# Kernel tuning notes

Measured on AMD Instinct MI355X. Metric: run time of the kernel, lower is better.

The kernel has to match this reference:

```python
import jax, jax.numpy as jnp
import numpy as np

S = 32   # parent grid side
G = 64   # child grid side (2*S)
C = 16   # channels
DN = ('NDHWC', 'DHWIO', 'NDHWC')


def conv3(t, w, b):
    # t: [D,H,W,Cin] dense grid; zero padding == nonexistent coords contribute 0 (ME semantics)
    return jax.lax.conv_general_dilated(t[None], w, (1, 1, 1), 'SAME', dimension_numbers=DN)[0] + b


def _grids():
    ix = jnp.arange(G)
    px = (ix % 2)[:, None, None]
    py = (ix % 2)[None, :, None]
    pz = (ix % 2)[None, None, :]
    oct_m = {(a, b, c): (px == a) & (py == b) & (pz == c)
             for a in (0, 1) for b in (0, 1) for c in (0, 1)}
    groups6 = [[(0, 0, 0)], [(1, 1, 0)], [(1, 0, 1)], [(0, 1, 1)],
               [(1, 0, 0), (0, 1, 0)], [(0, 0, 1), (1, 1, 1)]]
    g6 = [jnp.any(jnp.stack([oct_m[o] for o in g]), 0) for g in groups6]
    s3 = (ix // 2)[:, None, None] + (ix // 2)[None, :, None] + (ix // 2)[None, None, :]
    m3 = [(s3 % 3) == j for j in range(3)]  # 3-way repartition (group_mask_gen_par)
    return g6, m3


def coder(feat, occ, w1, b1, w2, b2):
    # ProbCoder: conv -> ReLU -> conv -> sigmoid; outputs exist only at input coords
    of = occ[..., None].astype(feat.dtype)
    h = jax.nn.relu(conv3(feat, w1, b1)) * of
    return jax.nn.sigmoid(conv3(h, w2, b2)) * of


def union(a, b):
    (fa, oa), (fb, ob) = a, b
    return (jnp.where(oa[..., None], fa, fb), oa | ob)


def _forward(x, w_down, b_down, w_fel1, b_fel1, w_fel2, b_fel2, w_up, b_up,
             wc1, bc1, wc2, bc2, wl1, bl1, wl2, bl2):
    g6, m3 = _grids()
    occ_x = x[..., 0] > 0                                    # GT occupied child voxels
    # down (stride-2 conv): coordinate effect only -- last_POV uses ones_like features
    p_occ = jnp.any(occ_x.reshape(S, 2, S, 2, S, 2), axis=(1, 3, 5))  # parent coords
    pf = p_occ[..., None].astype(x.dtype)                    # last_POV features (ones)
    # FEL (dfa): conv(1->C,k3)+ReLU+conv(C->C,k3), outputs only at existing parents
    h = jax.nn.relu(conv3(pf, w_fel1, b_fel1)) * pf
    h = conv3(h, w_fel2, b_fel2) * pf                        # [S,S,S,C]
    # generative transposed conv k2 s2: each parent emits 8 children (octant-specific weight)
    up = jnp.einsum('xyzc,ocd->xyzod', h, w_up) + b_up       # [S,S,S,8,C]
    up = up.reshape(S, S, S, 2, 2, 2, C).transpose(0, 3, 1, 4, 2, 5, 6).reshape(G, G, G, C)
    occ = jnp.repeat(jnp.repeat(jnp.repeat(p_occ, 2, 0), 2, 1), 2, 2)  # child coords of prob
    prob_f = up * occ[..., None]
    lab = [occ_x & g for g in g6]                            # generate_label: GT per group
    # ---------- anchor1 compression (3 sub-stages inside octant group 1) ----------
    a1_o = occ & g6[0]
    a1_f = prob_f * a1_o[..., None]
    r = [(a1_f * m[..., None], a1_o & m) for m in m3]
    lab1 = [lab[0] & m for m in m3]
    p11 = coder(r[0][0], r[0][1], wc1[0], bc1[0], wc2[0], bc2[0])
    d1s = (prob_f * lab1[0][..., None], lab1[0])             # decoded GT of sub-stage 1
    in2 = union(r[1], d1s)
    p12 = coder(in2[0], in2[1], wl1[0], bl1[0], wl2[0], bl2[0]) * (in2[1] & m3[1])[..., None]
    d2s = (prob_f * lab1[1][..., None], lab1[1])
    in3 = union(union(d1s, d2s), r[2])
    p13 = coder(in3[0], in3[1], wl1[1], bl1[1], wl2[1], bl2[1]) * (in3[1] & m3[2])[..., None]
    # ---------- anchors 2..6 ----------
    dec = (prob_f * lab[0][..., None], lab[0])               # prob_anchor1_dec
    probs = [p11, p12, p13]
    for k in range(1, 6):
        ak_o = occ & g6[k]
        ak = (prob_f * ak_o[..., None], ak_o)
        inp = union(dec, ak)
        pk = coder(inp[0], inp[1], wc1[k], bc1[k], wc2[k], bc2[k]) * (inp[1] & g6[k])[..., None]
        probs.append(pk)
        if k < 5:
            dk = (prob_f * lab[k][..., None], lab[k])
            dec = union(dec, dk)
    probs = jnp.stack([p[..., 0] for p in probs], 0)          # [8,G,G,G]
    labels = jnp.stack([lab1[0], lab1[1], lab1[2], lab[1], lab[2], lab[3], lab[4], lab[5]], 0).astype(x.dtype)
    return probs, labels


def setup_inputs() -> dict:
    key = jax.random.key(0)
    ks = jax.random.split(key, 20)
    f = lambda k, s: jax.random.normal(k, s, jnp.float32) * 0.1
    x = (jax.random.uniform(ks[0], (G, G, G, 1)) < 0.5).astype(jnp.float32)
    return {
        'x': x,
        'w_down': f(ks[1], (2, 2, 2, 1, 1)), 'b_down': f(ks[2], (1,)),
        'w_fel1': f(ks[3], (3, 3, 3, 1, C)), 'b_fel1': f(ks[4], (C,)),
        'w_fel2': f(ks[5], (3, 3, 3, C, C)), 'b_fel2': f(ks[6], (C,)),
        'w_up': f(ks[7], (8, C, C)), 'b_up': f(ks[8], (C,)),
        'wc1': f(ks[9], (6, 3, 3, 3, C, C)), 'bc1': f(ks[10], (6, C)),
        'wc2': f(ks[11], (6, 3, 3, 3, C, 1)), 'bc2': f(ks[12], (6, 1)),
        'wl1': f(ks[13], (2, 5, 5, 5, C, C)), 'bl1': f(ks[14], (2, C)),
        'wl2': f(ks[15], (2, 5, 5, 5, C, 1)), 'bl2': f(ks[16], (2, 1)),
    }


def reference(x, w_down, b_down, w_fel1, b_fel1, w_fel2, b_fel2, w_up, b_up,
              wc1, bc1, wc2, bc2, wl1, bl1, wl2, bl2):
    return _forward(x, w_down, b_down, w_fel1, b_fel1, w_fel2, b_fel2, w_up, b_up,
                    wc1, bc1, wc2, bc2, wl1, bl1, wl2, bl2)
```

## Files before the change

### kernel.cpp

```cpp
#include <hip/hip_runtime.h>
#include <cstdint>
#include <math.h>

#define G 64
#define S 32
#define G3 (G*G*G)
#define S3 (S*S*S)

typedef unsigned long long u64;
typedef unsigned int u32;
typedef unsigned short u16;

typedef __attribute__((ext_vector_type(8))) short s16x8;
typedef __attribute__((ext_vector_type(4))) float f32x4;

__device__ __forceinline__ float sigmoidf_(float v) {
    return 1.0f / (1.0f + expf(-v));
}
__device__ __forceinline__ u32 f2bf_rne(float f) {
    u32 u = __float_as_uint(f);
    u += 0x7fff + ((u >> 16) & 1);
    return u >> 16;
}
__device__ __forceinline__ u64 rfl64(u64 v) {
    u32 lo = __builtin_amdgcn_readfirstlane((u32)v);
    u32 hi = __builtin_amdgcn_readfirstlane((u32)(v >> 32));
    return ((u64)hi << 32) | lo;
}
__device__ __forceinline__ u64 tap_hit(u64 wout, u64 wn, int dz) {
    return (dz >= 0) ? (wout & (wn >> dz)) : (wout & (wn << (-dz)));
}

__global__ __launch_bounds__(256) void k_pocc(const float* __restrict__ x,
                                              unsigned char* __restrict__ pocc) {
    int p = blockIdx.x * 256 + threadIdx.x;
    if (p >= S3) return;
    int pz = p & 31, py = (p >> 5) & 31, px = p >> 10;
    const float* b = x + (((size_t)(px * 2) * G + py * 2) * G + pz * 2);
    bool occ = false;
    #pragma unroll
    for (int a = 0; a < 2; a++)
        #pragma unroll
        for (int bb = 0; bb < 2; bb++)
            #pragma unroll
            for (int c = 0; c < 2; c++)
                occ = occ || (b[((size_t)a * G + bb) * G + c] > 0.0f);
    pocc[p] = occ ? 1 : 0;
}

__global__ __launch_bounds__(256) void k_fel1(const unsigned char* __restrict__ pocc,
                                              const float* __restrict__ w1,
                                              const float* __restrict__ b1,
                                              float* __restrict__ h1) {
    int p = blockIdx.x * 256 + threadIdx.x;
    if (p >= S3) return;
    int pz = p & 31, py = (p >> 5) & 31, px = p >> 10;
    float* o = h1 + (size_t)p * 16;
    if (!pocc[p]) {
        #pragma unroll
        for (int i = 0; i < 16; i++) o[i] = 0.0f;
        return;
    }
    float acc[16];
    #pragma unroll
    for (int i = 0; i < 16; i++) acc[i] = b1[i];
    for (int dx = -1; dx <= 1; ++dx) {
        int nx = px + dx; if ((unsigned)nx >= S) continue;
        for (int dy = -1; dy <= 1; ++dy) {
            int ny = py + dy; if ((unsigned)ny >= S) continue;
            for (int dz = -1; dz <= 1; ++dz) {
                int nz = pz + dz; if ((unsigned)nz >= S) continue;
                if (pocc[(nx * S + ny) * S + nz]) {
                    const float* w = w1 + (((dx + 1) * 3 + (dy + 1)) * 3 + (dz + 1)) * 16;
                    #pragma unroll
                    for (int i = 0; i < 16; i++) acc[i] += w[i];
                }
            }
        }
    }
    #pragma unroll
    for (int i = 0; i < 16; i++) o[i] = fmaxf(acc[i], 0.0f);
}

__global__ __launch_bounds__(256) void k_fel2(const unsigned char* __restrict__ pocc,
                                              const float* __restrict__ h1,
                                              const float* __restrict__ w2,
                                              const float* __restrict__ b2,
                                              float* __restrict__ h2) {
    int p = blockIdx.x * 256 + threadIdx.x;
    if (p >= S3) return;
    int pz = p & 31, py = (p >> 5) & 31, px = p >> 10;
    float* o = h2 + (size_t)p * 16;
    if (!pocc[p]) {
        #pragma unroll
        for (int i = 0; i < 16; i++) o[i] = 0.0f;
        return;
    }
    float acc[16];
    #pragma unroll
    for (int i = 0; i < 16; i++) acc[i] = b2[i];
    for (int dx = -1; dx <= 1; ++dx) {
        int nx = px + dx; if ((unsigned)nx >= S) continue;
        for (int dy = -1; dy <= 1; ++dy) {
            int ny = py + dy; if ((unsigned)ny >= S) continue;
            for (int dz = -1; dz <= 1; ++dz) {
                int nz = pz + dz; if ((unsigned)nz >= S) continue;
                const float* f = h1 + (size_t)((nx * S + ny) * S + nz) * 16;
                const float* w = w2 + (((dx + 1) * 3 + (dy + 1)) * 3 + (dz + 1)) * 256;
                #pragma unroll
                for (int ci = 0; ci < 16; ++ci) {
                    float fv = f[ci];
                    #pragma unroll
                    for (int co = 0; co < 16; ++co)
                        acc[co] = fmaf(fv, w[ci * 16 + co], acc[co]);
                }
            }
        }
    }
    #pragma unroll
    for (int i = 0; i < 16; i++) o[i] = acc[i];
}

__global__ __launch_bounds__(256) void k_up(const unsigned char* __restrict__ pocc,
                                            const float* __restrict__ h2,
                                            const float* __restrict__ wup,
                                            const float* __restrict__ bup,
                                            u16* __restrict__ probf16) {
    int p = blockIdx.x * 256 + threadIdx.x;
    if (p >= S3) return;
    int pz = p & 31, py = (p >> 5) & 31, px = p >> 10;
    bool occ = pocc[p] != 0;
    float h[16];
    const float* hp = h2 + (size_t)p * 16;
    #pragma unroll
    for (int i = 0; i < 16; i++) h[i] = hp[i];
    #pragma unroll
    for (int o = 0; o < 8; o++) {
        int a = o >> 2, b = (o >> 1) & 1, c = o & 1;
        u16* op = probf16 + (((size_t)(2 * px + a) * G + (2 * py + b)) * G + (2 * pz + c)) * 16;
        uint4* o4 = reinterpret_cast<uint4*>(op);
        if (!occ) {
            o4[0] = make_uint4(0, 0, 0, 0);
            o4[1] = make_uint4(0, 0, 0, 0);
        } else {
            u32 pk[8];
            #pragma unroll
            for (int i = 0; i < 8; ++i) {
                float a0 = bup[2 * i], a1 = bup[2 * i + 1];
                #pragma unroll
                for (int cc = 0; cc < 16; cc++) {
                    a0 = fmaf(h[cc], wup[(o * 16 + cc) * 16 + 2 * i], a0);
                    a1 = fmaf(h[cc], wup[(o * 16 + cc) * 16 + 2 * i + 1], a1);
                }
                pk[i] = f2bf_rne(a0) | (f2bf_rne(a1) << 16);
            }
            o4[0] = make_uint4(pk[0], pk[1], pk[2], pk[3]);
            o4[1] = make_uint4(pk[4], pk[5], pk[6], pk[7]);
        }
    }
}

__global__ __launch_bounds__(256) void k_masks(const float* __restrict__ x,
                                               const unsigned char* __restrict__ pocc,
                                               u64* __restrict__ lw_in,
                                               u64* __restrict__ lw_fin,
                                               float* __restrict__ labels) {
    int z = threadIdx.x;
    int y = blockIdx.x * 4 + threadIdx.y;
    int xx = blockIdx.y;
    int v = (xx * G + y) * G + z;
    int par = ((xx & 1) << 2) | ((y & 1) << 1) | (z & 1);
    const int gmap[8] = {0, 5, 4, 3, 4, 2, 1, 5};
    int g = gmap[par];
    int t = ((xx >> 1) + (y >> 1) + (z >> 1)) % 3;
    bool occ = pocc[(((xx >> 1) * S) + (y >> 1)) * S + (z >> 1)] != 0;
    bool ox = x[v] > 0.0f;
    bool g0 = (g == 0);

    bool mi[8], mf[8], lb[8];
    mi[0] = occ && g0 && (t == 0);
    mi[1] = (occ && g0 && (t == 1)) || (ox && g0 && (t == 0));
    mi[2] = (ox && g0 && (t < 2)) || (occ && g0 && (t == 2));
    mi[3] = (ox && g0)       || (occ && (g == 1));
    mi[4] = (ox && (g <= 1)) || (occ && (g == 2));
    mi[5] = (ox && (g <= 2)) || (occ && (g == 3));
    mi[6] = (ox && (g <= 3)) || (occ && (g == 4));
    mi[7] = (ox && (g <= 4)) || (occ && (g == 5));

    mf[0] = occ && g0 && (t == 0);
    mf[1] = occ && g0 && (t == 1);
    mf[2] = occ && g0 && (t == 2);
    mf[3] = occ && (g == 1);
    mf[4] = occ && (g == 2);
    mf[5] = occ && (g == 3);
    mf[6] = occ && (g == 4);
    mf[7] = occ && (g == 5);

    lb[0] = ox && g0 && (t == 0);
    lb[1] = ox && g0 && (t == 1);
    lb[2] = ox && g0 && (t == 2);
    lb[3] = ox && (g == 1);
    lb[4] = ox && (g == 2);
    lb[5] = ox && (g == 3);
    lb[6] = ox && (g == 4);
    lb[7] = ox && (g == 5);

    int line = xx * G + y;
    #pragma unroll
    for (int c = 0; c < 8; ++c) {
        u64 wi = __ballot((int)mi[c]);
        u64 wf = __ballot((int)mf[c]);
        if (z == 0) {
            lw_in[c * 4096 + line] = wi;
            lw_fin[c * 4096 + line] = wf;
        }
        labels[(size_t)c * G3 + v] = lb[c] ? 1.0f : 0.0f;
    }
}

#define FRAGSTRIDE 38400
__global__ __launch_bounds__(64) void k_prep_bfrag(const float* __restrict__ wc1,
                                                   const float* __restrict__ wl1,
                                                   u16* __restrict__ bfrag) {
    int c = blockIdx.x;
    int frag = blockIdx.y;
    int lane = threadIdx.x;
    bool is5 = (c == 1 || c == 2);
    int R = is5 ? 2 : 1;
    int KS = 2 * R + 1;
    int npair = R + 1;
    int nfrag = KS * KS * npair;
    if (frag >= nfrag) return;
    const float* W = is5 ? (wl1 + (size_t)(c - 1) * 32000)
                         : (wc1 + (size_t)((c == 0) ? 0 : (c - 2)) * 6912);
    int dxdy = frag / npair, p = frag - dxdy * npair;
    int dxi = dxdy / KS, dyi = dxdy - dxi * KS;
    int dziA = 2 * p, dziB = 2 * p + 1;
    int co = lane & 15, kg = lane >> 4;
    u16 outv[8];
    #pragma unroll
    for (int j = 0; j < 8; ++j) {
        int k = kg * 8 + j;
        int ci = k & 15;
        int dzi = (k < 16) ? dziA : dziB;
        float v = 0.0f;
        if (dzi < KS)
            v = W[(size_t)((dxi * KS + dyi) * KS + dzi) * 256 + ci * 16 + co];
        outv[j] = (u16)f2bf_rne(v);
    }
    u16* o = bfrag + (size_t)c * FRAGSTRIDE + ((size_t)frag * 64 + lane) * 8;
    uint4 pk;
    pk.x = outv[0] | ((u32)outv[1] << 16);
    pk.y = outv[2] | ((u32)outv[3] << 16);
    pk.z = outv[4] | ((u32)outv[5] << 16);
    pk.w = outv[6] | ((u32)outv[7] << 16);
    *reinterpret_cast<uint4*>(o) = pk;
}

__global__ __launch_bounds__(256) void k_conv1_mfma(const u16* __restrict__ probf16,
                                                    const u64* __restrict__ lw_in,
                                                    const u16* __restrict__ bfrag,
                                                    const float* __restrict__ bc1,
                                                    const float* __restrict__ bl1,
                                                    u16* __restrict__ hbase,
                                                    int coderBase) {
    int c = coderBase + blockIdx.y;
    bool is5 = (c == 1 || c == 2);
    int R = is5 ? 2 : 1;
    int KS = 2 * R + 1, npair = R + 1;
    const u64* lw = lw_in + (size_t)c * 4096;
    u16* h_c = hbase + (size_t)blockIdx.y * G3 * 16;
    const u16* bf = bfrag + (size_t)c * FRAGSTRIDE;
    const float* bptr = is5 ? (bl1 + (c - 1) * 16)
                            : (bc1 + ((c == 0) ? 0 : (c - 2)) * 16);

    int x = blockIdx.x >> 4;
    int y0 = (blockIdx.x & 15) << 2;
    int w = threadIdx.y;
    int lane = threadIdx.x;
    int yw = y0 + w;

    u64 w0 = rfl64(lw[x * G + yw]);
    u64 anyw = lw[x * G + y0] | lw[x * G + y0 + 1] | lw[x * G + y0 + 2] | lw[x * G + y0 + 3];
    if (anyw == 0ULL) return;

    __shared__ u32 lds[8 * 2304 / 4];

    int col = lane & 15, kg = lane >> 4;
    float bv = bptr[col];
    f32x4 acc[4];
    #pragma unroll
    for (int s = 0; s < 4; ++s) acc[s] = (f32x4){bv, bv, bv, bv};

    int nlines = 4 + 2 * R;
    int nunits = nlines * 144;
    int t = w * 64 + lane;

    for (int dx = -R; dx <= R; ++dx) {
        int nx = x + dx;
        __syncthreads();
        if ((unsigned)nx < G) {
            for (int u = t; u < nunits; u += 256) {
                int s = u / 144; int q = u - s * 144;
                int lz = q >> 1, half = q & 1;
                int gz = lz - 4;
                int ny = y0 - R + s;
                uint4 val = make_uint4(0, 0, 0, 0);
                if ((unsigned)ny < G && (unsigned)gz < G) {
                    u64 wn = lw[nx * G + ny];
                    if ((wn >> gz) & 1)
                        val = *reinterpret_cast<const uint4*>(
                            probf16 + ((size_t)((nx * G + ny) * G + gz) * 16 + half * 8));
                }
                *reinterpret_cast<uint4*>(
                    reinterpret_cast<char*>(lds) + s * 2304 + half * 1152 + lz * 16) = val;
            }
        }
        __syncthreads();
        if (w0 == 0ULL || (unsigned)nx >= G) continue;

        for (int dy = -R; dy <= R; ++dy) {
            int ny = yw + dy;
            if ((unsigned)ny >= G) continue;
            u64 wn = rfl64(lw[nx * G + ny]);
            if (wn == 0ULL) continue;
            int slot = w + dy + R;
            for (int p = 0; p < npair; ++p) {
                int dzA = -R + 2 * p;
                int dzB = dzA + 1;
                bool hasB = (dzB <= R);
                u64 hit = tap_hit(w0, wn, dzA);
                if (hasB) hit |= tap_hit(w0, wn, dzB);
                if (hit == 0ULL) continue;
                int frag = ((dx + R) * KS + (dy + R)) * npair + p;
                s16x8 bf8 = *reinterpret_cast<const s16x8*>(bf + ((size_t)frag * 64 + lane) * 8);
                int dz = (kg < 2) ? dzA : (hasB ? dzB : dzA);
                int lzb = (lane & 15) + dz + 4;
                const char* abase = reinterpret_cast<const char*>(lds)
                                    + slot * 2304 + (kg & 1) * 1152;
                #pragma unroll
                for (int s = 0; s < 4; ++s) {
                    if (((hit >> (s * 16)) & 0xFFFFULL) == 0ULL) continue;
                    s16x8 a = *reinterpret_cast<const s16x8*>(abase + (s * 16 + lzb) * 16);
                    acc[s] = __builtin_amdgcn_mfma_f32_16x16x32_bf16(a, bf8, acc[s], 0, 0, 0);
                }
            }
        }
    }

    if (w0 == 0ULL) return;
    u16* hline = h_c + (size_t)(x * G + yw) * G * 16;
    #pragma unroll
    for (int s = 0; s < 4; ++s) {
        #pragma unroll
        for (int r = 0; r < 4; ++r) {
            int z = s * 16 + kg * 4 + r;
            if ((w0 >> z) & 1) {
                float v = fmaxf(acc[s][r], 0.0f);
                hline[z * 16 + col] = (u16)f2bf_rne(v);
            }
        }
    }
}

template <int KS>
__device__ __forceinline__ void conv2_body(const u32* __restrict__ h_c,
                                           const u64* __restrict__ lwi,
                                           const u64* __restrict__ lwf,
                                           const float* __restrict__ w2,
                                           const float* __restrict__ b2,
                                           float* __restrict__ outp) {
    const int R = KS / 2;
    int z = threadIdx.x;
    int line = blockIdx.x * 4 + threadIdx.y;
    int xx = line >> 6, y = line & 63;
    int v = (xx * G + y) * G + z;
    u64 wf = rfl64(lwf[line]);
    if (wf == 0ULL) { outp[v] = 0.0f; return; }
    bool m = (wf >> z) & 1;

    float acc = b2[0];
    for (int dx = -R; dx <= R; ++dx) {
        int nx = xx + dx; if ((unsigned)nx >= G) continue;
        for (int dy = -R; dy <= R; ++dy) {
            int ny = y + dy; if ((unsigned)ny >= G) continue;
            u64 wn = rfl64(lwi[nx * G + ny]);
            if (wn == 0ULL) continue;
            const float* wbase = w2 + (size_t)(((dx + R) * KS + (dy + R)) * KS) * 16;
            #pragma unroll
            for (int dz = -R; dz <= R; ++dz) {
                if (tap_hit(wf, wn, dz) == 0ULL) continue;
                int nz = z + dz;
                bool ok = (unsigned)nz < G;
                int nzc = ok ? nz : 0;
                bool mn = ok && ((wn >> nzc) & 1);
                const float* w = wbase + (dz + R) * 16;
                if (mn) {
                    const uint4* h4 = reinterpret_cast<const uint4*>(
                        h_c + ((size_t)((nx * G + ny) * G + nzc)) * 8);
                    uint4 Ua = h4[0], Ub = h4[1];
                    u32 uu[8] = {Ua.x, Ua.y, Ua.z, Ua.w, Ub.x, Ub.y, Ub.z, Ub.w};
                    #pragma unroll
                    for (int i = 0; i < 8; ++i) {
                        float lo = __uint_as_float(uu[i] << 16);
                        float hi = __uint_as_float(uu[i] & 0xffff0000u);
                        acc = fmaf(lo, w[2 * i], acc);
                        acc = fmaf(hi, w[2 * i + 1], acc);
                    }
                }
            }
        }
    }
    outp[v] = m ? sigmoidf_(acc) : 0.0f;
}

__global__ __launch_bounds__(256) void k_conv2_all(const u32* __restrict__ hbase,
                                                   const u64* __restrict__ lw_in,
                                                   const u64* __restrict__ lw_fin,
                                                   const float* __restrict__ wc2,
                                                   const float* __restrict__ bc2,
                                                   const float* __restrict__ wl2,
                                                   const float* __restrict__ bl2,
                                                   float* __restrict__ out,
                                                   int coderBase) {
    int c = coderBase + blockIdx.y;
    const u64* lwi = lw_in + (size_t)c * 4096;
    const u64* lwf = lw_fin + (size_t)c * 4096;
    const u32* h_c = hbase + (size_t)blockIdx.y * G3 * 8;
    float* outp = out + (size_t)c * G3;
    if (c == 1 || c == 2) {
        conv2_body<5>(h_c, lwi, lwf, wl2 + (size_t)(c - 1) * 2000, bl2 + (c - 1), outp);
    } else {
        int j = (c == 0) ? 0 : (c - 2);
        conv2_body<3>(h_c, lwi, lwf, wc2 + (size_t)j * 432, bc2 + j, outp);
    }
}

extern "C" void kernel_launch(void* const* d_in, const int* in_sizes, int n_in,
                              void* d_out, int out_size, void* d_ws, size_t ws_size,
                              hipStream_t stream) {
    const float* x      = (const float*)d_in[0];
    const float* w_fel1 = (const float*)d_in[3];
    const float* b_fel1 = (const float*)d_in[4];
    const float* w_fel2 = (const float*)d_in[5];
    const float* b_fel2 = (const float*)d_in[6];
    const float* w_up   = (const float*)d_in[7];
    const float* b_up   = (const float*)d_in[8];
    const float* wc1    = (const float*)d_in[9];
    const float* bc1    = (const float*)d_in[10];
    const float* wc2    = (const float*)d_in[11];
    const float* bc2    = (const float*)d_in[12];
    const float* wl1    = (const float*)d_in[13];
    const float* bl1    = (const float*)d_in[14];
    const float* wl2    = (const float*)d_in[15];
    const float* bl2    = (const float*)d_in[16];
    float* out = (float*)d_out;

    char* ws = (char*)d_ws;
    u16*  probf16 = (u16*)(ws);
    float* h1     = (float*)(ws + 8388608);
    float* h2     = (float*)(ws + 10485760);
    unsigned char* pocc = (unsigned char*)(ws + 12582912);
    u64* lw_in  = (u64*)(ws + 12615680);
    u64* lw_fin = (u64*)(ws + 12877824);
    u16* bfrag  = (u16*)(ws + 13139968);
    u16* hbase  = (u16*)(ws + 13754368);

    const size_t fixed_end = 13754368;
    const size_t hsz = (size_t)G3 * 16 * 2;
    int B = 2;
    if (fixed_end + 8 * hsz <= ws_size) B = 8;
    else if (fixed_end + 4 * hsz <= ws_size) B = 4;

    k_pocc <<<dim3(S3 / 256), dim3(256), 0, stream>>>(x, pocc);
    k_fel1 <<<dim3(S3 / 256), dim3(256), 0, stream>>>(pocc, w_fel1, b_fel1, h1);
    k_fel2 <<<dim3(S3 / 256), dim3(256), 0, stream>>>(pocc, h1, w_fel2, b_fel2, h2);
    k_up   <<<dim3(S3 / 256), dim3(256), 0, stream>>>(pocc, h2, w_up, b_up, probf16);
    k_masks<<<dim3(16, 64), dim3(64, 4), 0, stream>>>(x, pocc, lw_in, lw_fin, out + (size_t)8 * G3);
    k_prep_bfrag<<<dim3(8, 75), dim3(64), 0, stream>>>(wc1, wl1, bfrag);

    for (int b0 = 0; b0 < 8; b0 += B) {
        int nb = (8 - b0 < B) ? (8 - b0) : B;
        k_conv1_mfma<<<dim3(1024, nb), dim3(64, 4), 0, stream>>>(
            probf16, lw_in, bfrag, bc1, bl1, hbase, b0);
        k_conv2_all<<<dim3(1024, nb), dim3(64, 4), 0, stream>>>(
            (const u32*)hbase, lw_in, lw_fin, wc2, bc2, wl2, bl2, out, b0);
    }
}
```

Before: 212.1 us.

## Read conv1 inputs directly from z-padded global buffer instead of LDS staging

The child probability features are now stored with four zero-padding voxels on each end of every z-line, so conv1 can load MFMA A-operands straight from global memory and mask them per lane with the neighbour occupancy bits. This removes the per-dx LDS staging loop and its two __syncthreads per step. The kernel is also templated on the kernel radius so the tap loops fully unroll, and each wave now exits early on its own empty line. The cost is more global/L2 traffic from overlapping neighbour reads and a slightly larger workspace.

```diff
diff --git a/kernel.cpp b/kernel.cpp
--- a/kernel.cpp
+++ b/kernel.cpp
@@ -14,6 +14,9 @@
 typedef __attribute__((ext_vector_type(8))) short s16x8;
 typedef __attribute__((ext_vector_type(4))) float f32x4;
 
+#define ZPAD 4
+#define ZSTR 72
+
 __device__ __forceinline__ float sigmoidf_(float v) {
     return 1.0f / (1.0f + expf(-v));
 }
@@ -26,6 +29,9 @@
     u32 lo = __builtin_amdgcn_readfirstlane((u32)v);
     u32 hi = __builtin_amdgcn_readfirstlane((u32)(v >> 32));
     return ((u64)hi << 32) | lo;
+}
+__device__ __forceinline__ u64 shiftw(u64 w, int dz) {
+    return (dz >= 0) ? (w >> dz) : (w << (-dz));
 }
 __device__ __forceinline__ u64 tap_hit(u64 wout, u64 wn, int dz) {
     return (dz >= 0) ? (wout & (wn >> dz)) : (wout & (wn << (-dz)));
@@ -125,7 +131,7 @@
                                             const float* __restrict__ h2,
                                             const float* __restrict__ wup,
                                             const float* __restrict__ bup,
-                                            u16* __restrict__ probf16) {
+                                            u16* __restrict__ pf) {
     int p = blockIdx.x * 256 + threadIdx.x;
     if (p >= S3) return;
     int pz = p & 31, py = (p >> 5) & 31, px = p >> 10;
@@ -137,7 +143,7 @@
     #pragma unroll
     for (int o = 0; o < 8; o++) {
         int a = o >> 2, b = (o >> 1) & 1, c = o & 1;
-        u16* op = probf16 + (((size_t)(2 * px + a) * G + (2 * py + b)) * G + (2 * pz + c)) * 16;
+        u16* op = pf + (((size_t)(2 * px + a) * G + (2 * py + b)) * ZSTR + (2 * pz + c) + ZPAD) * 16;
         uint4* o4 = reinterpret_cast<uint4*>(op);
         if (!occ) {
             o4[0] = make_uint4(0, 0, 0, 0);
@@ -157,6 +163,22 @@
             o4[0] = make_uint4(pk[0], pk[1], pk[2], pk[3]);
             o4[1] = make_uint4(pk[4], pk[5], pk[6], pk[7]);
         }
+    }
+    if (pz == 0) {
+        uint4 zz = make_uint4(0, 0, 0, 0);
+        #pragma unroll
+        for (int a = 0; a < 2; a++)
+            #pragma unroll
+            for (int b = 0; b < 2; b++) {
+                u16* lp = pf + ((size_t)((2 * px + a) * G + (2 * py + b)) * ZSTR) * 16;
+                #pragma unroll
+                for (int q = 0; q < ZPAD; q++) {
+                    *reinterpret_cast<uint4*>(lp + q * 16) = zz;
+                    *reinterpret_cast<uint4*>(lp + q * 16 + 8) = zz;
+                    *reinterpret_cast<uint4*>(lp + (G + ZPAD + q) * 16) = zz;
+                    *reinterpret_cast<uint4*>(lp + (G + ZPAD + q) * 16 + 8) = zz;
+                }
+            }
     }
 }
 
@@ -257,7 +279,83 @@
     *reinterpret_cast<uint4*>(o) = pk;
 }
 
-__global__ __launch_bounds__(256) void k_conv1_mfma(const u16* __restrict__ probf16,
+template <int R>
+__device__ __forceinline__ void conv1_mfma_body(const u16* __restrict__ pf,
+                                                const u64* __restrict__ lw,
+                                                const u16* __restrict__ bf,
+                                                const float* __restrict__ bptr,
+                                                u16* __restrict__ h_c) {
+    const int KS = 2 * R + 1, NP = R + 1;
+    int lane = threadIdx.x;
+    int line = blockIdx.x * 4 + threadIdx.y;
+    int x = line >> 6, y = line & 63;
+
+    u64 w0 = rfl64(lw[line]);
+    if (w0 == 0ULL) return;
+
+    int m = lane & 15, kg = lane >> 4, half = kg & 1;
+    float bv = bptr[m];
+    f32x4 acc[4];
+    #pragma unroll
+    for (int s = 0; s < 4; ++s) acc[s] = (f32x4){bv, bv, bv, bv};
+    const s16x8 zf = {};
+
+    for (int dx = -R; dx <= R; ++dx) {
+        int nx = x + dx;
+        if ((unsigned)nx >= G) continue;
+        u64 wrow[KS];
+        #pragma unroll
+        for (int dy = -R; dy <= R; ++dy) {
+            int ny = y + dy;
+            wrow[dy + R] = ((unsigned)ny < G) ? rfl64(lw[nx * G + ny]) : 0ULL;
+        }
+        #pragma unroll
+        for (int dy = -R; dy <= R; ++dy) {
+            u64 wn = wrow[dy + R];
+            if (wn == 0ULL) continue;
+            int ny = y + dy;
+            const u16* nb = pf + ((size_t)(nx * G + ny)) * ZSTR * 16;
+            #pragma unroll
+            for (int p = 0; p < NP; ++p) {
+                const int dzA = -R + 2 * p;
+                const int dzB = dzA + 1;
+                const bool hasB = (dzB <= R);
+                u64 wshA = shiftw(wn, dzA);
+                u64 wshB = hasB ? shiftw(wn, dzB) : wshA;
+                u64 hit = (w0 & wshA) | (hasB ? (w0 & wshB) : 0ULL);
+                if (hit == 0ULL) continue;
+                int frag = ((dx + R) * KS + (dy + R)) * NP + p;
+                s16x8 b8 = *reinterpret_cast<const s16x8*>(bf + ((size_t)frag * 64 + lane) * 8);
+                u64 wsh_l = (kg < 2) ? wshA : wshB;
+                int dz_l = (kg < 2) ? dzA : (hasB ? dzB : dzA);
+                const u16* ab = nb + (size_t)(ZPAD + dz_l + m) * 16 + half * 8;
+                #pragma unroll
+                for (int s = 0; s < 4; ++s) {
+                    if (((hit >> (s * 16)) & 0xFFFFULL) == 0ULL) continue;
+                    s16x8 a = *reinterpret_cast<const s16x8*>(ab + s * 256);
+                    u32 mb = (u32)(wsh_l >> (s * 16 + m)) & 1u;
+                    a = mb ? a : zf;
+                    acc[s] = __builtin_amdgcn_mfma_f32_16x16x32_bf16(a, b8, acc[s], 0, 0, 0);
+                }
+            }
+        }
+    }
+
+    u16* hline = h_c + (size_t)line * G * 16;
+    #pragma unroll
+    for (int s = 0; s < 4; ++s) {
+        #pragma unroll
+        for (int r = 0; r < 4; ++r) {
+            int z = s * 16 + kg * 4 + r;
+            if ((w0 >> z) & 1) {
+                float v = fmaxf(acc[s][r], 0.0f);
+                hline[z * 16 + m] = (u16)f2bf_rne(v);
+            }
+        }
+    }
+}
+
+__global__ __launch_bounds__(256) void k_conv1_mfma(const u16* __restrict__ pf,
                                                     const u64* __restrict__ lw_in,
                                                     const u16* __restrict__ bfrag,
                                                     const float* __restrict__ bc1,
@@ -265,101 +363,14 @@
                                                     u16* __restrict__ hbase,
                                                     int coderBase) {
     int c = coderBase + blockIdx.y;
-    bool is5 = (c == 1 || c == 2);
-    int R = is5 ? 2 : 1;
-    int KS = 2 * R + 1, npair = R + 1;
     const u64* lw = lw_in + (size_t)c * 4096;
     u16* h_c = hbase + (size_t)blockIdx.y * G3 * 16;
     const u16* bf = bfrag + (size_t)c * FRAGSTRIDE;
-    const float* bptr = is5 ? (bl1 + (c - 1) * 16)
-                            : (bc1 + ((c == 0) ? 0 : (c - 2)) * 16);
-
-    int x = blockIdx.x >> 4;
-    int y0 = (blockIdx.x & 15) << 2;
-    int w = threadIdx.y;
-    int lane = threadIdx.x;
-    int yw = y0 + w;
-
-    u64 w0 = rfl64(lw[x * G + yw]);
-    u64 anyw = lw[x * G + y0] | lw[x * G + y0 + 1] | lw[x * G + y0 + 2] | lw[x * G + y0 + 3];
-    if (anyw == 0ULL) return;
-
-    __shared__ u32 lds[8 * 2304 / 4];
-
-    int col = lane & 15, kg = lane >> 4;
-    float bv = bptr[col];
-    f32x4 acc[4];
-    #pragma unroll
-    for (int s = 0; s < 4; ++s) acc[s] = (f32x4){bv, bv, bv, bv};
-
-    int nlines = 4 + 2 * R;
-    int nunits = nlines * 144;
-    int t = w * 64 + lane;
-
-    for (int dx = -R; dx <= R; ++dx) {
-        int nx = x + dx;
-        __syncthreads();
-        if ((unsigned)nx < G) {
-            for (int u = t; u < nunits; u += 256) {
-                int s = u / 144; int q = u - s * 144;
-                int lz = q >> 1, half = q & 1;
-                int gz = lz - 4;
-                int ny = y0 - R + s;
-                uint4 val = make_uint4(0, 0, 0, 0);
-                if ((unsigned)ny < G && (unsigned)gz < G) {
-                    u64 wn = lw[nx * G + ny];
-                    if ((wn >> gz) & 1)
-                        val = *reinterpret_cast<const uint4*>(
-                            probf16 + ((size_t)((nx * G + ny) * G + gz) * 16 + half * 8));
-                }
-                *reinterpret_cast<uint4*>(
-                    reinterpret_cast<char*>(lds) + s * 2304 + half * 1152 + lz * 16) = val;
-            }
-        }
-        __syncthreads();
-        if (w0 == 0ULL || (unsigned)nx >= G) continue;
-
-        for (int dy = -R; dy <= R; ++dy) {
-            int ny = yw + dy;
-            if ((unsigned)ny >= G) continue;
-            u64 wn = rfl64(lw[nx * G + ny]);
-            if (wn == 0ULL) continue;
-            int slot = w + dy + R;
-            for (int p = 0; p < npair; ++p) {
-                int dzA = -R + 2 * p;
-                int dzB = dzA + 1;
-                bool hasB = (dzB <= R);
-                u64 hit = tap_hit(w0, wn, dzA);
-                if (hasB) hit |= tap_hit(w0, wn, dzB);
-                if (hit == 0ULL) continue;
-                int frag = ((dx + R) * KS + (dy + R)) * npair + p;
-                s16x8 bf8 = *reinterpret_cast<const s16x8*>(bf + ((size_t)frag * 64 + lane) * 8);
-                int dz = (kg < 2) ? dzA : (hasB ? dzB : dzA);
-                int lzb = (lane & 15) + dz + 4;
-                const char* abase = reinterpret_cast<const char*>(lds)
-                                    + slot * 2304 + (kg & 1) * 1152;
-                #pragma unroll
-                for (int s = 0; s < 4; ++s) {
-                    if (((hit >> (s * 16)) & 0xFFFFULL) == 0ULL) continue;
-                    s16x8 a = *reinterpret_cast<const s16x8*>(abase + (s * 16 + lzb) * 16);
-                    acc[s] = __builtin_amdgcn_mfma_f32_16x16x32_bf16(a, bf8, acc[s], 0, 0, 0);
-                }
-            }
-        }
-    }
-
-    if (w0 == 0ULL) return;
-    u16* hline = h_c + (size_t)(x * G + yw) * G * 16;
-    #pragma unroll
-    for (int s = 0; s < 4; ++s) {
-        #pragma unroll
-        for (int r = 0; r < 4; ++r) {
-            int z = s * 16 + kg * 4 + r;
-            if ((w0 >> z) & 1) {
-                float v = fmaxf(acc[s][r], 0.0f);
-                hline[z * 16 + col] = (u16)f2bf_rne(v);
-            }
-        }
+    if (c == 1 || c == 2) {
+        conv1_mfma_body<2>(pf, lw, bf, bl1 + (c - 1) * 16, h_c);
+    } else {
+        int j = (c == 0) ? 0 : (c - 2);
+        conv1_mfma_body<1>(pf, lw, bf, bc1 + j * 16, h_c);
     }
 }
 
@@ -458,15 +469,15 @@
 
     char* ws = (char*)d_ws;
     u16*  probf16 = (u16*)(ws);
-    float* h1     = (float*)(ws + 8388608);
-    float* h2     = (float*)(ws + 10485760);
-    unsigned char* pocc = (unsigned char*)(ws + 12582912);
-    u64* lw_in  = (u64*)(ws + 12615680);
-    u64* lw_fin = (u64*)(ws + 12877824);
-    u16* bfrag  = (u16*)(ws + 13139968);
-    u16* hbase  = (u16*)(ws + 13754368);
-
-    const size_t fixed_end = 13754368;
+    float* h1     = (float*)(ws + 9437184);
+    float* h2     = (float*)(ws + 11534336);
+    unsigned char* pocc = (unsigned char*)(ws + 13631488);
+    u64* lw_in  = (u64*)(ws + 13664256);
+    u64* lw_fin = (u64*)(ws + 13926400);
+    u16* bfrag  = (u16*)(ws + 14188544);
+    u16* hbase  = (u16*)(ws + 14802944);
+
+    const size_t fixed_end = 14802944;
     const size_t hsz = (size_t)G3 * 16 * 2;
     int B = 2;
     if (fixed_end + 8 * hsz <= ws_size) B = 8;
```

Result: slower. 299.6 us (+41.2%).
